# Performance work log

Measured on AMD Instinct MI355X. Metric: run time of the kernel, lower is better.

## Reference

```python
import jax, jax.numpy as jnp
import numpy as np

K = 9      # kernel_size
H = 6      # num_head
HD = 64    # head_dim
D = H * HD # reduced_hidden_dim = 384
B, S = 16, 1024
OUT = 384  # hidden_dim // 2


def setup_inputs() -> dict:
    key = jax.random.key(0)
    k = jax.random.split(key, 5)
    q = jax.random.normal(k[0], (B, S, D), dtype=jnp.float32)
    ks = jax.random.normal(k[1], (B, S, D), dtype=jnp.float32)
    v = jax.random.normal(k[2], (B, S, D), dtype=jnp.float32)
    Wk = jax.random.normal(k[3], (K * H, D), dtype=jnp.float32) * 0.02
    bk = jnp.zeros((K * H,), dtype=jnp.float32)
    Wp = jax.random.normal(k[4], (OUT, D), dtype=jnp.float32) * 0.02
    bp = jnp.zeros((OUT,), dtype=jnp.float32)
    return {"q": q, "ks": ks, "v": v, "Wk": Wk, "bk": bk, "Wp": Wp, "bp": bp}


def reference(q, ks, v, Wk, bk, Wp, bp):
    b, s, d = v.shape
    pad = K // 2
    # expand4conv: zero-pad along seq and gather K-wide sliding windows
    vp = jnp.pad(v, ((0, 0), (pad, pad), (0, 0)))            # [B, S+K-1, D]
    win = jnp.stack([vp[:, i:i + s] for i in range(K)], -1)  # [B, S, D, K]
    win = win.reshape(b, s, H, HD, K)                        # [B, S, H, HD, K]
    # dynamic kernel: softmax over kernel taps
    logits = jnp.einsum('bsd,od->bso', q * ks, Wk) + bk       # [B, S, K*H]
    dk = jax.nn.softmax(logits.reshape(b, s, H, K), axis=-1)  # [B, S, H, K]
    # local weighted reduction over the window
    out = jnp.einsum('bshdk,bshk->bshd', win, dk).reshape(b, s, d)
    return jnp.einsum('bsd,od->bso', out, Wp) + bp            # [B, S, OUT]
```

## Files before the change

### kernel.cpp

```cpp
#include <hip/hip_runtime.h>
#include <hip/hip_bf16.h>

#define BB 16
#define SS 1024
#define DD 384
#define HH 6
#define KK 9
#define KH 54
#define OUTD 384
#define NKT 12
#define VLD 392

typedef __attribute__((ext_vector_type(4))) float floatx4;
typedef __attribute__((ext_vector_type(8))) __bf16 bf16x8;
typedef __attribute__((ext_vector_type(4))) __bf16 bf16x4;

__global__ __launch_bounds__(256) void cast_kernel(const float* __restrict__ Wk,
                                                   const float* __restrict__ Wp,
                                                   __bf16* __restrict__ WkT,
                                                   __bf16* __restrict__ WpT) {
    int i = blockIdx.x * 256 + threadIdx.x;
    if (i < 4 * NKT * 64 * 8) {
        int e = i & 7, lane = (i >> 3) & 63, t = i >> 9;
        int kstep = t % NKT, ntile = t / NKT;
        int row = ntile * 16 + (lane & 15);
        int col = kstep * 32 + ((lane >> 4) << 3) + e;
        WkT[i] = (row < KH) ? (__bf16)Wk[row * DD + col] : (__bf16)0.0f;
    } else if (i < 24576 + 24 * NKT * 64 * 8) {
        int j = i - 24576;
        int e = j & 7, lane = (j >> 3) & 63, t = j >> 9;
        int kstep = t % NKT, ntile = t / NKT;
        int row = ntile * 16 + (lane & 15);
        int col = kstep * 32 + ((lane >> 4) << 3) + e;
        WpT[j] = (__bf16)Wp[row * DD + col];
    }
}

__global__ __launch_bounds__(256) void fused_kernel(const float* __restrict__ q,
                                                    const float* __restrict__ ks,
                                                    const float* __restrict__ v,
                                                    const __bf16* __restrict__ WkT,
                                                    const float* __restrict__ bk,
                                                    const __bf16* __restrict__ WpT,
                                                    const float* __restrict__ bp,
                                                    float* __restrict__ out) {
    __shared__ __bf16 vqS[40 * VLD];
    __shared__ float  dkS[32 * 56];
    __shared__ __align__(16) char uS[32 * VLD * 2];
    float*  lgS = (float*)uS;
    __bf16* aS  = (__bf16*)uS;

    const int tid  = threadIdx.x;
    const int wave = tid >> 6;
    const int lane = tid & 63;
    const int m0   = blockIdx.x * 32;
    const int b    = blockIdx.x >> 5;
    const int s0   = (blockIdx.x & 31) * 32;
    const int fr   = lane & 15;
    const int fk   = (lane >> 4) * 8;
    const int col_in = lane & 15;
    const int rgrp   = (lane >> 4) * 4;

    {
        const float* qb = q  + (size_t)m0 * DD;
        const float* kb = ks + (size_t)m0 * DD;
#pragma unroll
        for (int it = 0; it < 12; ++it) {
            int c = tid + it * 256;
            int row = c / 96, col = (c % 96) * 4;
            floatx4 qv = *reinterpret_cast<const floatx4*>(qb + (size_t)row * DD + col);
            floatx4 kv = *reinterpret_cast<const floatx4*>(kb + (size_t)row * DD + col);
            floatx4 pr = qv * kv;
            bf16x4 pk = { (__bf16)pr.x, (__bf16)pr.y, (__bf16)pr.z, (__bf16)pr.w };
            *reinterpret_cast<bf16x4*>(&vqS[row * VLD + col]) = pk;
        }
    }
    __syncthreads();

    {
        const int wml = (wave & 1) * 16;
        const int kh  = wave >> 1;
        floatx4 acc[4] = {};
#pragma unroll
        for (int s = 0; s < 6; ++s) {
            int kst = kh * 6 + s;
            bf16x8 af = *reinterpret_cast<const bf16x8*>(&vqS[(wml + fr) * VLD + kst * 32 + fk]);
#pragma unroll
            for (int j = 0; j < 4; ++j) {
                bf16x8 bf = *reinterpret_cast<const bf16x8*>(
                    WkT + (((j * NKT + kst) * 64 + lane) << 3));
                acc[j] = __builtin_amdgcn_mfma_f32_16x16x32_bf16(af, bf, acc[j], 0, 0, 0);
            }
        }
#pragma unroll
        for (int j = 0; j < 4; ++j)
#pragma unroll
            for (int r = 0; r < 4; ++r)
                lgS[(kh * 32 + wml + rgrp + r) * 66 + j * 16 + col_in] = acc[j][r];
    }
    __syncthreads();

    if (tid < 32 * HH) {
        int row = tid / HH, h = tid % HH;
        float lg[KK];
        float mx = -1e30f;
#pragma unroll
        for (int k = 0; k < KK; ++k) {
            int o = h * KK + k;
            float s = lgS[row * 66 + o] + lgS[(32 + row) * 66 + o] + bk[o];
            lg[k] = s;
            mx = fmaxf(mx, s);
        }
        float sum = 0.0f;
#pragma unroll
        for (int k = 0; k < KK; ++k) { lg[k] = __expf(lg[k] - mx); sum += lg[k]; }
        float inv = 1.0f / sum;
#pragma unroll
        for (int k = 0; k < KK; ++k) dkS[row * 56 + h * KK + k] = lg[k] * inv;
    }
    {
        const float* vb = v + (size_t)b * SS * DD;
#pragma unroll
        for (int it = 0; it < 15; ++it) {
            int c = tid + it * 256;
            int row = c / 96, col = (c % 96) * 4;
            int r = s0 + row - 4;
            floatx4 val = {};
            if (r >= 0 && r < SS)
                val = *reinterpret_cast<const floatx4*>(vb + (size_t)r * DD + col);
            bf16x4 vk = { (__bf16)val.x, (__bf16)val.y, (__bf16)val.z, (__bf16)val.w };
            *reinterpret_cast<bf16x4*>(&vqS[row * VLD + col]) = vk;
        }
    }
    __syncthreads();

#pragma unroll
    for (int it = 0; it < 12; ++it) {
        int p = tid + it * 256;
        int row = p / 96, c4 = p % 96;
        int h = c4 >> 4;
        const float* dkr = &dkS[row * 56 + h * KK];
        floatx4 a = {};
#pragma unroll
        for (int k = 0; k < KK; ++k) {
            bf16x4 w = *reinterpret_cast<const bf16x4*>(&vqS[(row + k) * VLD + c4 * 4]);
            floatx4 wf = { (float)w[0], (float)w[1], (float)w[2], (float)w[3] };
            a += wf * dkr[k];
        }
        bf16x4 o = { (__bf16)a.x, (__bf16)a.y, (__bf16)a.z, (__bf16)a.w };
        *reinterpret_cast<bf16x4*>(&aS[row * VLD + c4 * 4]) = o;
    }
    __syncthreads();

    {
        const int wm  = (wave & 1) * 16;
        const int nt0 = (wave >> 1) * 12;
        floatx4 acc[12] = {};
#pragma unroll 2
        for (int s = 0; s < NKT; ++s) {
            bf16x8 af = *reinterpret_cast<const bf16x8*>(&aS[(wm + fr) * VLD + s * 32 + fk]);
#pragma unroll
            for (int j = 0; j < 12; ++j) {
                bf16x8 bf = *reinterpret_cast<const bf16x8*>(
                    WpT + ((((nt0 + j) * NKT + s) * 64 + lane) << 3));
                acc[j] = __builtin_amdgcn_mfma_f32_16x16x32_bf16(af, bf, acc[j], 0, 0, 0);
            }
        }
        float* ob = out + (size_t)m0 * OUTD;
#pragma unroll
        for (int j = 0; j < 12; ++j) {
            int col = (nt0 + j) * 16 + col_in;
            float bv = bp[col];
#pragma unroll
            for (int r = 0; r < 4; ++r)
                ob[(size_t)(wm + rgrp + r) * OUTD + col] = acc[j][r] + bv;
        }
    }
}

extern "C" void kernel_launch(void* const* d_in, const int* in_sizes, int n_in,
                              void* d_out, int out_size, void* d_ws, size_t ws_size,
                              hipStream_t stream) {
    const float* q  = (const float*)d_in[0];
    const float* ks = (const float*)d_in[1];
    const float* v  = (const float*)d_in[2];
    const float* Wk = (const float*)d_in[3];
    const float* bk = (const float*)d_in[4];
    const float* Wp = (const float*)d_in[5];
    const float* bp = (const float*)d_in[6];
    float* out = (float*)d_out;

    __bf16* WkT = (__bf16*)d_ws;
    __bf16* WpT = (__bf16*)((char*)d_ws + 49152);

    cast_kernel<<<(24576 + 147456 + 255) / 256, 256, 0, stream>>>(Wk, Wp, WkT, WpT);
    fused_kernel<<<(BB * SS) / 32, 256, 0, stream>>>(q, ks, v, WkT, bk, WpT, bp, out);
}
```

Baseline: 130.1 us.

## Halve row tile to 16 rows per block and remap waves over output tiles

```diff
diff --git a/kernel.cpp b/kernel.cpp
--- a/kernel.cpp
+++ b/kernel.cpp
@@ -36,26 +36,26 @@
     }
 }
 
-__global__ __launch_bounds__(256) void fused_kernel(const float* __restrict__ q,
-                                                    const float* __restrict__ ks,
-                                                    const float* __restrict__ v,
-                                                    const __bf16* __restrict__ WkT,
-                                                    const float* __restrict__ bk,
-                                                    const __bf16* __restrict__ WpT,
-                                                    const float* __restrict__ bp,
-                                                    float* __restrict__ out) {
-    __shared__ __bf16 vqS[40 * VLD];
-    __shared__ float  dkS[32 * 56];
-    __shared__ __align__(16) char uS[32 * VLD * 2];
+__global__ __launch_bounds__(256, 4) void fused_kernel(const float* __restrict__ q,
+                                                       const float* __restrict__ ks,
+                                                       const float* __restrict__ v,
+                                                       const __bf16* __restrict__ WkT,
+                                                       const float* __restrict__ bk,
+                                                       const __bf16* __restrict__ WpT,
+                                                       const float* __restrict__ bp,
+                                                       float* __restrict__ out) {
+    __shared__ __bf16 vqS[24 * VLD];
+    __shared__ float  dkS[16 * 56];
+    __shared__ __align__(16) char uS[16 * VLD * 2];
     float*  lgS = (float*)uS;
     __bf16* aS  = (__bf16*)uS;
 
     const int tid  = threadIdx.x;
     const int wave = tid >> 6;
     const int lane = tid & 63;
-    const int m0   = blockIdx.x * 32;
-    const int b    = blockIdx.x >> 5;
-    const int s0   = (blockIdx.x & 31) * 32;
+    const int m0   = blockIdx.x * 16;
+    const int b    = blockIdx.x >> 6;
+    const int s0   = (blockIdx.x & 63) * 16;
     const int fr   = lane & 15;
     const int fk   = (lane >> 4) * 8;
     const int col_in = lane & 15;
@@ -65,7 +65,7 @@
         const float* qb = q  + (size_t)m0 * DD;
         const float* kb = ks + (size_t)m0 * DD;
 #pragma unroll
-        for (int it = 0; it < 12; ++it) {
+        for (int it = 0; it < 6; ++it) {
             int c = tid + it * 256;
             int row = c / 96, col = (c % 96) * 4;
             floatx4 qv = *reinterpret_cast<const floatx4*>(qb + (size_t)row * DD + col);
@@ -78,36 +78,27 @@
     __syncthreads();
 
     {
-        const int wml = (wave & 1) * 16;
-        const int kh  = wave >> 1;
-        floatx4 acc[4] = {};
-#pragma unroll
-        for (int s = 0; s < 6; ++s) {
-            int kst = kh * 6 + s;
-            bf16x8 af = *reinterpret_cast<const bf16x8*>(&vqS[(wml + fr) * VLD + kst * 32 + fk]);
-#pragma unroll
-            for (int j = 0; j < 4; ++j) {
-                bf16x8 bf = *reinterpret_cast<const bf16x8*>(
-                    WkT + (((j * NKT + kst) * 64 + lane) << 3));
-                acc[j] = __builtin_amdgcn_mfma_f32_16x16x32_bf16(af, bf, acc[j], 0, 0, 0);
-            }
-        }
-#pragma unroll
-        for (int j = 0; j < 4; ++j)
-#pragma unroll
-            for (int r = 0; r < 4; ++r)
-                lgS[(kh * 32 + wml + rgrp + r) * 66 + j * 16 + col_in] = acc[j][r];
-    }
-    __syncthreads();
-
-    if (tid < 32 * HH) {
+        floatx4 acc = {};
+#pragma unroll
+        for (int s = 0; s < NKT; ++s) {
+            bf16x8 af = *reinterpret_cast<const bf16x8*>(&vqS[fr * VLD + s * 32 + fk]);
+            bf16x8 bf = *reinterpret_cast<const bf16x8*>(
+                WkT + (((wave * NKT + s) * 64 + lane) << 3));
+            acc = __builtin_amdgcn_mfma_f32_16x16x32_bf16(af, bf, acc, 0, 0, 0);
+        }
+#pragma unroll
+        for (int r = 0; r < 4; ++r)
+            lgS[(rgrp + r) * 66 + wave * 16 + col_in] = acc[r];
+    }
+    __syncthreads();
+
+    if (tid < 16 * HH) {
         int row = tid / HH, h = tid % HH;
         float lg[KK];
         float mx = -1e30f;
 #pragma unroll
         for (int k = 0; k < KK; ++k) {
-            int o = h * KK + k;
-            float s = lgS[row * 66 + o] + lgS[(32 + row) * 66 + o] + bk[o];
+            float s = lgS[row * 66 + h * KK + k] + bk[h * KK + k];
             lg[k] = s;
             mx = fmaxf(mx, s);
         }
@@ -118,24 +109,37 @@
 #pragma unroll
         for (int k = 0; k < KK; ++k) dkS[row * 56 + h * KK + k] = lg[k] * inv;
     }
+
     {
         const float* vb = v + (size_t)b * SS * DD;
-#pragma unroll
-        for (int it = 0; it < 15; ++it) {
-            int c = tid + it * 256;
-            int row = c / 96, col = (c % 96) * 4;
-            int r = s0 + row - 4;
-            floatx4 val = {};
-            if (r >= 0 && r < SS)
-                val = *reinterpret_cast<const floatx4*>(vb + (size_t)r * DD + col);
-            bf16x4 vk = { (__bf16)val.x, (__bf16)val.y, (__bf16)val.z, (__bf16)val.w };
-            *reinterpret_cast<bf16x4*>(&vqS[row * VLD + col]) = vk;
-        }
-    }
-    __syncthreads();
-
-#pragma unroll
-    for (int it = 0; it < 12; ++it) {
+        if (s0 != 0 && s0 != SS - 16) {
+#pragma unroll
+            for (int it = 0; it < 9; ++it) {
+                int c = tid + it * 256;
+                int row = c / 96, col = (c % 96) * 4;
+                floatx4 val = *reinterpret_cast<const floatx4*>(
+                    vb + (size_t)(s0 + row - 4) * DD + col);
+                bf16x4 vk = { (__bf16)val.x, (__bf16)val.y, (__bf16)val.z, (__bf16)val.w };
+                *reinterpret_cast<bf16x4*>(&vqS[row * VLD + col]) = vk;
+            }
+        } else {
+#pragma unroll
+            for (int it = 0; it < 9; ++it) {
+                int c = tid + it * 256;
+                int row = c / 96, col = (c % 96) * 4;
+                int r = s0 + row - 4;
+                floatx4 val = {};
+                if (r >= 0 && r < SS)
+                    val = *reinterpret_cast<const floatx4*>(vb + (size_t)r * DD + col);
+                bf16x4 vk = { (__bf16)val.x, (__bf16)val.y, (__bf16)val.z, (__bf16)val.w };
+                *reinterpret_cast<bf16x4*>(&vqS[row * VLD + col]) = vk;
+            }
+        }
+    }
+    __syncthreads();
+
+#pragma unroll
+    for (int it = 0; it < 6; ++it) {
         int p = tid + it * 256;
         int row = p / 96, c4 = p % 96;
         int h = c4 >> 4;
@@ -153,14 +157,13 @@
     __syncthreads();
 
     {
-        const int wm  = (wave & 1) * 16;
-        const int nt0 = (wave >> 1) * 12;
-        floatx4 acc[12] = {};
-#pragma unroll 2
+        const int nt0 = wave * 6;
+        floatx4 acc[6] = {};
+#pragma unroll
         for (int s = 0; s < NKT; ++s) {
-            bf16x8 af = *reinterpret_cast<const bf16x8*>(&aS[(wm + fr) * VLD + s * 32 + fk]);
-#pragma unroll
-            for (int j = 0; j < 12; ++j) {
+            bf16x8 af = *reinterpret_cast<const bf16x8*>(&aS[fr * VLD + s * 32 + fk]);
+#pragma unroll
+            for (int j = 0; j < 6; ++j) {
                 bf16x8 bf = *reinterpret_cast<const bf16x8*>(
                     WpT + ((((nt0 + j) * NKT + s) * 64 + lane) << 3));
                 acc[j] = __builtin_amdgcn_mfma_f32_16x16x32_bf16(af, bf, acc[j], 0, 0, 0);
@@ -168,12 +171,12 @@
         }
         float* ob = out + (size_t)m0 * OUTD;
 #pragma unroll
-        for (int j = 0; j < 12; ++j) {
+        for (int j = 0; j < 6; ++j) {
             int col = (nt0 + j) * 16 + col_in;
             float bv = bp[col];
 #pragma unroll
             for (int r = 0; r < 4; ++r)
-                ob[(size_t)(wm + rgrp + r) * OUTD + col] = acc[j][r] + bv;
+                ob[(size_t)(rgrp + r) * OUTD + col] = acc[j][r] + bv;
         }
     }
 }
@@ -194,5 +197,5 @@
     __bf16* WpT = (__bf16*)((char*)d_ws + 49152);
 
     cast_kernel<<<(24576 + 147456 + 255) / 256, 256, 0, stream>>>(Wk, Wp, WkT, WpT);
-    fused_kernel<<<(BB * SS) / 32, 256, 0, stream>>>(q, ks, v, WkT, bk, WpT, bp, out);
+    fused_kernel<<<(BB * SS) / 16, 256, 0, stream>>>(q, ks, v, WkT, bk, WpT, bp, out);
 }
```

Result: faster. 126.7 us (-2.6%).
